# Kernel tuning notes

Hardware: AMD Instinct MI355X
Metric: run time of the kernel (lower is better)

## Reference

```python
import jax, jax.numpy as jnp
import numpy as np

B, T, C = 1, 4096, 2048
NH, HS, NQG = 16, 128, 4          # n_head, head_size, n_query_groups (GQA)
Q_PER_KV = NH // NQG              # 4
QKV_DIM = (NH + 2 * NQG) * HS     # 3072
ROT = HS // 2                     # rotary half-dim = 64


def setup_inputs() -> dict:
    key = jax.random.key(0)
    k0, k1, k2 = jax.random.split(key, 3)
    x = jax.random.normal(k0, (B, T, C), dtype=jnp.float32)
    W_attn = jax.random.normal(k1, (QKV_DIM, C), dtype=jnp.float32) * 0.02
    W_proj = jax.random.normal(k2, (C, C), dtype=jnp.float32) * 0.02
    # RoPE cache: cos/sin of shape (T, head_size/2), flash-attn convention
    inv_freq = 1.0 / (10000.0 ** (jnp.arange(0, HS, 2, dtype=jnp.float32) / HS))
    freqs = jnp.arange(T, dtype=jnp.float32)[:, None] * inv_freq[None, :]
    return {"x": x, "cos": jnp.cos(freqs), "sin": jnp.sin(freqs),
            "W_attn": W_attn, "W_proj": W_proj}


def _apply_rope(t, cos, sin):
    # t: (B, T, H, HS); cos/sin: (T, ROT). Non-interleaved (rotate-half) form.
    x1, x2 = t[..., :ROT], t[..., ROT:]
    c = cos[None, :, None, :]
    s = sin[None, :, None, :]
    return jnp.concatenate([x1 * c - x2 * s, x2 * c + x1 * s], axis=-1)


def reference(x, cos, sin, W_attn, W_proj):
    Bx, Tx, Cx = x.shape
    qkv = jnp.einsum('btc,fc->btf', x, W_attn)                 # (B,T,3072)
    qkv = qkv.reshape(Bx, Tx, NQG, Q_PER_KV + 2, HS)
    q = qkv[:, :, :, :Q_PER_KV, :].reshape(Bx, Tx, NH, HS)     # (B,T,16,128)
    k = qkv[:, :, :, Q_PER_KV, :]                              # (B,T,4,128)
    v = qkv[:, :, :, Q_PER_KV + 1, :]                          # (B,T,4,128)
    q = _apply_rope(q, cos, sin)
    k = _apply_rope(k, cos, sin)
    # GQA: expand kv groups to match query heads (repeat_interleave on head dim)
    k = jnp.repeat(k, Q_PER_KV, axis=2)                        # (B,T,16,128)
    v = jnp.repeat(v, Q_PER_KV, axis=2)
    scale = 1.0 / np.sqrt(HS).astype(np.float32)
    scores = jnp.einsum('bthd,bshd->bhts', q, k) * scale       # (B,H,T,T)
    causal = jnp.tril(jnp.ones((Tx, Tx), dtype=bool))
    scores = jnp.where(causal[None, None], scores, jnp.finfo(scores.dtype).min)
    attn = jax.nn.softmax(scores, axis=-1)
    y = jnp.einsum('bhts,bshd->bthd', attn, v).reshape(Bx, Tx, Cx)
    return jnp.einsum('btc,oc->bto', y, W_proj)
```

## Files before the change

kernel.cpp:

```cpp
#include <hip/hip_runtime.h>
#include <hip/hip_bf16.h>

typedef __hip_bfloat16 bf16;
typedef __attribute__((ext_vector_type(8))) short short8;
typedef __attribute__((ext_vector_type(4))) short short4v;
typedef __attribute__((ext_vector_type(4))) float floatx4;

#define T_SEQ 4096
#define C_DIM 2048
#define NHEAD 16
#define HSZ   128
#define NGRP  4

#define MFMA_BF16(A,B,C) __builtin_amdgcn_mfma_f32_16x16x32_bf16((A),(B),(C),0,0,0)

__device__ __forceinline__ void gld_lds16(const bf16* g, bf16* l) {
  __builtin_amdgcn_global_load_lds(
      (__attribute__((address_space(1))) void*)(g),
      (__attribute__((address_space(3))) void*)(l), 16, 0, 0);
}

__global__ void cvt_kernel(const float* __restrict__ src, bf16* __restrict__ dst, long n)
{
  const long i = ((long)blockIdx.x * blockDim.x + threadIdx.x) * 8;
  if (i >= n) return;
  const float4 a = *(const float4*)(src + i);
  const float4 b = *(const float4*)(src + i + 4);
  bf16 tmp[8];
  tmp[0] = __float2bfloat16(a.x); tmp[1] = __float2bfloat16(a.y);
  tmp[2] = __float2bfloat16(a.z); tmp[3] = __float2bfloat16(a.w);
  tmp[4] = __float2bfloat16(b.x); tmp[5] = __float2bfloat16(b.y);
  tmp[6] = __float2bfloat16(b.z); tmp[7] = __float2bfloat16(b.w);
  *(short8*)(dst + i) = *(const short8*)tmp;
}

__global__ __launch_bounds__(256, 2)
void gemm_bt_kernel(const bf16* __restrict__ A, const bf16* __restrict__ B,
                    float* __restrict__ Cf, bf16* __restrict__ Cq,
                    bf16* __restrict__ Ck, bf16* __restrict__ Cvt,
                    int K, int qkv_mode)
{
  __shared__ alignas(16) bf16 As[128 * 64];
  __shared__ alignas(16) bf16 Bs[128 * 64];

  const int t  = threadIdx.x;
  const int w  = t >> 6, l = t & 63;
  const int wr = w >> 1, wc = w & 1;
  const int q4 = l >> 4, ln = l & 15;
  const long bm = (long)blockIdx.y * 128;
  const long bn = (long)blockIdx.x * 128;

  floatx4 acc[4][4] = {};

  const bf16* Ab = A + (bm + t / 8) * (long)K + (t % 8) * 8;
  const bf16* Bb = B + (bn + t / 8) * (long)K + (t % 8) * 8;

  for (int k0 = 0; k0 < K; k0 += 64) {
    __syncthreads();
#pragma unroll
    for (int i = 0; i < 4; ++i) {
      gld_lds16(Ab + (long)i * 32 * K + k0, As + (i * 256 + w * 64) * 8);
      gld_lds16(Bb + (long)i * 32 * K + k0, Bs + (i * 256 + w * 64) * 8);
    }
    __syncthreads();
#pragma unroll
    for (int kk = 0; kk < 64; kk += 32) {
      short8 af[4], bfr[4];
      const int co = kk + q4 * 8;
#pragma unroll
      for (int mi = 0; mi < 4; ++mi)
        af[mi] = *(const short8*)(As + (wr * 64 + mi * 16 + ln) * 64 + co);
#pragma unroll
      for (int ni = 0; ni < 4; ++ni)
        bfr[ni] = *(const short8*)(Bs + (wc * 64 + ni * 16 + ln) * 64 + co);
#pragma unroll
      for (int mi = 0; mi < 4; ++mi)
#pragma unroll
        for (int ni = 0; ni < 4; ++ni)
          acc[mi][ni] = MFMA_BF16(af[mi], bfr[ni], acc[mi][ni]);
    }
  }

  if (!qkv_mode) {
#pragma unroll
    for (int mi = 0; mi < 4; ++mi) {
      const long r0 = bm + wr * 64 + mi * 16 + q4 * 4;
#pragma unroll
      for (int ni = 0; ni < 4; ++ni) {
        const long c = bn + wc * 64 + ni * 16 + ln;
#pragma unroll
        for (int r = 0; r < 4; ++r)
          Cf[(r0 + r) * C_DIM + c] = acc[mi][ni][r];
      }
    }
  } else {
    const int cb = blockIdx.x;
    const int g = cb / 6, slot = cb - g * 6;
    if (slot == 5) {
      bf16* dstv = Cvt + (long)g * HSZ * T_SEQ;
#pragma unroll
      for (int mi = 0; mi < 4; ++mi) {
        const long r0 = bm + wr * 64 + mi * 16 + q4 * 4;
#pragma unroll
        for (int ni = 0; ni < 4; ++ni) {
          const long c = wc * 64 + ni * 16 + ln;
          short4v pk;
#pragma unroll
          for (int r = 0; r < 4; ++r) {
            bf16 v = __float2bfloat16(acc[mi][ni][r]);
            pk[r] = *(short*)&v;
          }
          *(short4v*)(dstv + c * T_SEQ + r0) = pk;
        }
      }
    } else {
      bf16* dst = (slot < 4) ? (Cq + (long)(g * 4 + slot) * T_SEQ * HSZ)
                             : (Ck + (long)g * T_SEQ * HSZ);
#pragma unroll
      for (int mi = 0; mi < 4; ++mi) {
        const long r0 = bm + wr * 64 + mi * 16 + q4 * 4;
#pragma unroll
        for (int ni = 0; ni < 4; ++ni) {
          const long c = wc * 64 + ni * 16 + ln;
#pragma unroll
          for (int r = 0; r < 4; ++r)
            dst[(r0 + r) * HSZ + c] = __float2bfloat16(acc[mi][ni][r]);
        }
      }
    }
  }
}

__global__ void rope_kernel(bf16* __restrict__ Q, bf16* __restrict__ Kb,
                            const float* __restrict__ cs, const float* __restrict__ sn)
{
  const long idx = (long)blockIdx.x * blockDim.x + threadIdx.x;
  const long NQ = (long)NHEAD * T_SEQ * 64;
  bf16* buf; long rem; float qs;
  if (idx < NQ) { buf = Q;  rem = idx;      qs = 0.08838834764831845f * 1.4426950408889634f; }
  else          { buf = Kb; rem = idx - NQ; qs = 1.0f; }
  const int d  = (int)(rem & 63);
  const int tt = (int)((rem >> 6) & (T_SEQ - 1));
  const int hh = (int)(rem >> 18);
  const float c = cs[tt * 64 + d];
  const float s = sn[tt * 64 + d];
  bf16* p = buf + ((long)hh * T_SEQ + tt) * HSZ + d;
  const float x1 = __bfloat162float(p[0]);
  const float x2 = __bfloat162float(p[64]);
  p[0]  = __float2bfloat16((x1 * c - x2 * s) * qs);
  p[64] = __float2bfloat16((x2 * c + x1 * s) * qs);
}

__global__ __launch_bounds__(512, 1)
void attn_kernel(const bf16* __restrict__ Qg, const bf16* __restrict__ Kg,
                 const bf16* __restrict__ Vtg, bf16* __restrict__ Y)
{
  __shared__ alignas(16) bf16 Ks[2][64][132];
  __shared__ alignas(16) bf16 Vt[2][128][68];
  __shared__ alignas(16) bf16 Ps[128][68];

  const int h = blockIdx.y;
  const int g = h >> 2;
  const int t = threadIdx.x;
  const int w = t >> 6, l = t & 63;
  const int q4 = l >> 4, ln = l & 15;

  const bf16* Qh = Qg + (long)h * T_SEQ * HSZ;
  const bf16* Kh = Kg + (long)g * T_SEQ * HSZ;
  const bf16* Vh = Vtg + (long)g * HSZ * T_SEQ;

  const int kr0 = t >> 4, kc = (t & 15) * 8;
  const int vr0 = t >> 3, vc = (t & 7) * 8;

  short8 ones_f;
#pragma unroll
  for (int i = 0; i < 8; ++i) ones_f[i] = (ln == 0) ? (short)0x3F80 : (short)0;

#pragma unroll 1
  for (int ph = 0; ph < 2; ++ph) {
    const int p = ph ? (31 - blockIdx.x) : blockIdx.x;
    const int qbase = p * 128 + w * 16;
    const int jmax = 2 * p + 1;

    short8 qf[4];
    {
      const long row = qbase + ln;
#pragma unroll
      for (int ks = 0; ks < 4; ++ks)
        qf[ks] = *(const short8*)(Qh + row * HSZ + ks * 32 + q4 * 8);
    }

    floatx4 acc[8] = {};
    floatx4 acc_l = {};

    short8 kpre[2], vpre[2];
#pragma unroll
    for (int i = 0; i < 2; ++i) {
      kpre[i] = *(const short8*)(Kh + (long)(kr0 + 32 * i) * HSZ + kc);
      vpre[i] = *(const short8*)(Vh + (long)(vr0 + 64 * i) * T_SEQ + vc);
    }
    __syncthreads();
#pragma unroll
    for (int i = 0; i < 2; ++i) {
      *(short8*)(&Ks[0][kr0 + 32 * i][kc]) = kpre[i];
      *(short8*)(&Vt[0][vr0 + 64 * i][vc]) = vpre[i];
    }
#pragma unroll
    for (int i = 0; i < 2; ++i) {
      kpre[i] = *(const short8*)(Kh + (long)(64 + kr0 + 32 * i) * HSZ + kc);
      vpre[i] = *(const short8*)(Vh + (long)(vr0 + 64 * i) * T_SEQ + 64 + vc);
    }

#pragma unroll 1
    for (int j = 0; j <= jmax; ++j) {
      const int s0 = j * 64;
      const int cur = j & 1;
      __syncthreads();

      if (j < jmax) {
        const int nxt = cur ^ 1;
#pragma unroll
        for (int i = 0; i < 2; ++i) {
          *(short8*)(&Ks[nxt][kr0 + 32 * i][kc]) = kpre[i];
          *(short8*)(&Vt[nxt][vr0 + 64 * i][vc]) = vpre[i];
        }
        if (j + 1 < jmax) {
          const int s2 = s0 + 128;
#pragma unroll
          for (int i = 0; i < 2; ++i) {
            kpre[i] = *(const short8*)(Kh + (long)(s2 + kr0 + 32 * i) * HSZ + kc);
            vpre[i] = *(const short8*)(Vh + (long)(vr0 + 64 * i) * T_SEQ + s2 + vc);
          }
        }
      }

      floatx4 sacc[4] = {};
#pragma unroll
      for (int ks = 0; ks < 4; ++ks) {
        short8 kf[4];
#pragma unroll
        for (int ni = 0; ni < 4; ++ni)
          kf[ni] = *(const short8*)(&Ks[cur][ni * 16 + ln][ks * 32 + q4 * 8]);
#pragma unroll
        for (int ni = 0; ni < 4; ++ni)
          sacc[ni] = MFMA_BF16(qf[ks], kf[ni], sacc[ni]);
      }

      {
        const int base_m = qbase + q4 * 4 - s0 - ln;
#pragma unroll
        for (int ni = 0; ni < 4; ++ni)
#pragma unroll
          for (int r = 0; r < 4; ++r) {
            float pv = __builtin_amdgcn_exp2f(sacc[ni][r]);
            if (base_m + r - ni * 16 < 0) pv = 0.f;
            Ps[w * 16 + q4 * 4 + r][ni * 16 + ln] = __float2bfloat16(pv);
          }
      }

#pragma unroll
      for (int ks = 0; ks < 2; ++ks) {
        short8 pf, vf[8];
        pf = *(const short8*)(&Ps[w * 16 + ln][ks * 32 + q4 * 8]);
#pragma unroll
        for (int nd = 0; nd < 8; ++nd)
          vf[nd] = *(const short8*)(&Vt[cur][nd * 16 + ln][ks * 32 + q4 * 8]);
        acc_l = MFMA_BF16(pf, ones_f, acc_l);
#pragma unroll
        for (int nd = 0; nd < 8; ++nd)
          acc[nd] = MFMA_BF16(pf, vf[nd], acc[nd]);
      }
    }

#pragma unroll
    for (int r = 0; r < 4; ++r) {
      const float lv = __shfl(acc_l[r], l & 48, 64);
      const float inv = (lv > 0.f) ? 1.f / lv : 0.f;
      const long tq = qbase + q4 * 4 + r;
#pragma unroll
      for (int nd = 0; nd < 8; ++nd)
        Y[tq * C_DIM + h * HSZ + nd * 16 + ln] = __float2bfloat16(acc[nd][r] * inv);
    }
  }
}

extern "C" void kernel_launch(void* const* d_in, const int* in_sizes, int n_in,
                              void* d_out, int out_size, void* d_ws, size_t ws_size,
                              hipStream_t stream)
{
  const float* x  = (const float*)d_in[0];
  const float* cs = (const float*)d_in[1];
  const float* sn = (const float*)d_in[2];
  const float* Wa = (const float*)d_in[3];
  const float* Wp = (const float*)d_in[4];
  float* out = (float*)d_out;

  const long nx  = (long)T_SEQ * C_DIM;
  const long nwa = (long)(NHEAD + 2 * NGRP) * HSZ * C_DIM;
  const long nwp = (long)C_DIM * C_DIM;
  const long nqh = (long)NHEAD * T_SEQ * HSZ;
  const long nkg = (long)NGRP * T_SEQ * HSZ;

  const size_t need = (size_t)(nx + nwa + nqh + 2 * nkg + nqh) * sizeof(bf16);
  if (ws_size < need) return;

  bf16* xb  = (bf16*)d_ws;
  bf16* Wab = xb + nx;
  bf16* Q   = Wab + nwa;
  bf16* K   = Q + nqh;
  bf16* Vt  = K + nkg;
  bf16* Y   = Vt + nkg;
  bf16* Wpb = xb;

  cvt_kernel<<<(int)(nx  / 8 / 256), 256, 0, stream>>>(x,  xb,  nx);
  cvt_kernel<<<(int)(nwa / 8 / 256), 256, 0, stream>>>(Wa, Wab, nwa);
  gemm_bt_kernel<<<dim3(24, 32), 256, 0, stream>>>(xb, Wab, nullptr, Q, K, Vt, C_DIM, 1);
  rope_kernel<<<20480, 256, 0, stream>>>(Q, K, cs, sn);
  attn_kernel<<<dim3(16, NHEAD), 512, 0, stream>>>(Q, K, Vt, Y);
  cvt_kernel<<<(int)(nwp / 8 / 256), 256, 0, stream>>>(Wp, Wpb, nwp);
  gemm_bt_kernel<<<dim3(16, 32), 256, 0, stream>>>(Y, Wpb, out, nullptr, nullptr, nullptr, C_DIM, 0);
}
```

Measured before the change: 351.7 us.

## Load K fragments directly from global memory instead of staging in LDS

```diff
diff --git a/kernel.cpp b/kernel.cpp
--- a/kernel.cpp
+++ b/kernel.cpp
@@ -151,13 +151,13 @@
   p[64] = __float2bfloat16((x2 * c + x1 * s) * qs);
 }
 
-__global__ __launch_bounds__(512, 1)
+__global__ __launch_bounds__(512, 2)
 void attn_kernel(const bf16* __restrict__ Qg, const bf16* __restrict__ Kg,
                  const bf16* __restrict__ Vtg, bf16* __restrict__ Y)
 {
-  __shared__ alignas(16) bf16 Ks[2][64][132];
   __shared__ alignas(16) bf16 Vt[2][128][68];
   __shared__ alignas(16) bf16 Ps[128][68];
+  __shared__ bf16 lds_pad[16384];
 
   const int h = blockIdx.y;
   const int g = h >> 2;
@@ -165,11 +165,12 @@
   const int w = t >> 6, l = t & 63;
   const int q4 = l >> 4, ln = l & 15;
 
+  if (Y == nullptr) lds_pad[t] = (bf16)0.f;
+
   const bf16* Qh = Qg + (long)h * T_SEQ * HSZ;
   const bf16* Kh = Kg + (long)g * T_SEQ * HSZ;
   const bf16* Vh = Vtg + (long)g * HSZ * T_SEQ;
 
-  const int kr0 = t >> 4, kc = (t & 15) * 8;
   const int vr0 = t >> 3, vc = (t & 7) * 8;
 
   short8 ones_f;
@@ -193,23 +194,17 @@
     floatx4 acc[8] = {};
     floatx4 acc_l = {};
 
-    short8 kpre[2], vpre[2];
-#pragma unroll
-    for (int i = 0; i < 2; ++i) {
-      kpre[i] = *(const short8*)(Kh + (long)(kr0 + 32 * i) * HSZ + kc);
+    short8 vpre[2];
+#pragma unroll
+    for (int i = 0; i < 2; ++i)
       vpre[i] = *(const short8*)(Vh + (long)(vr0 + 64 * i) * T_SEQ + vc);
-    }
     __syncthreads();
 #pragma unroll
-    for (int i = 0; i < 2; ++i) {
-      *(short8*)(&Ks[0][kr0 + 32 * i][kc]) = kpre[i];
+    for (int i = 0; i < 2; ++i)
       *(short8*)(&Vt[0][vr0 + 64 * i][vc]) = vpre[i];
-    }
-#pragma unroll
-    for (int i = 0; i < 2; ++i) {
-      kpre[i] = *(const short8*)(Kh + (long)(64 + kr0 + 32 * i) * HSZ + kc);
+#pragma unroll
+    for (int i = 0; i < 2; ++i)
       vpre[i] = *(const short8*)(Vh + (long)(vr0 + 64 * i) * T_SEQ + 64 + vc);
-    }
 
 #pragma unroll 1
     for (int j = 0; j <= jmax; ++j) {
@@ -220,30 +215,30 @@
       if (j < jmax) {
         const int nxt = cur ^ 1;
 #pragma unroll
-        for (int i = 0; i < 2; ++i) {
-          *(short8*)(&Ks[nxt][kr0 + 32 * i][kc]) = kpre[i];
+        for (int i = 0; i < 2; ++i)
           *(short8*)(&Vt[nxt][vr0 + 64 * i][vc]) = vpre[i];
-        }
         if (j + 1 < jmax) {
           const int s2 = s0 + 128;
 #pragma unroll
-          for (int i = 0; i < 2; ++i) {
-            kpre[i] = *(const short8*)(Kh + (long)(s2 + kr0 + 32 * i) * HSZ + kc);
+          for (int i = 0; i < 2; ++i)
             vpre[i] = *(const short8*)(Vh + (long)(vr0 + 64 * i) * T_SEQ + s2 + vc);
-          }
         }
       }
 
       floatx4 sacc[4] = {};
-#pragma unroll
-      for (int ks = 0; ks < 4; ++ks) {
-        short8 kf[4];
-#pragma unroll
-        for (int ni = 0; ni < 4; ++ni)
-          kf[ni] = *(const short8*)(&Ks[cur][ni * 16 + ln][ks * 32 + q4 * 8]);
-#pragma unroll
-        for (int ni = 0; ni < 4; ++ni)
-          sacc[ni] = MFMA_BF16(qf[ks], kf[ni], sacc[ni]);
+      {
+        const bf16* Kt = Kh + (long)s0 * HSZ;
+        short8 kf[4][4];
+#pragma unroll
+        for (int ks = 0; ks < 4; ++ks)
+#pragma unroll
+          for (int ni = 0; ni < 4; ++ni)
+            kf[ks][ni] = *(const short8*)(Kt + (long)(ni * 16 + ln) * HSZ + ks * 32 + q4 * 8);
+#pragma unroll
+        for (int ks = 0; ks < 4; ++ks)
+#pragma unroll
+          for (int ni = 0; ni < 4; ++ni)
+            sacc[ni] = MFMA_BF16(qf[ks], kf[ks][ni], sacc[ni]);
       }
 
       {
```

After: 544.0 us. 54.7% more time.
